# Kernel tuning notes

Hardware: AMD Instinct MI355X
Metric: run time of the kernel (lower is better)

## Reference

```python
import jax, jax.numpy as jnp
import numpy as np
from jax.scipy.stats import norm as jnorm

B, S, D, H, E, K, FF = 8, 256, 1024, 16, 4, 2, 4096
HD = D // H
NOISE_EPS = 0.01
LOSS_COEF = 0.01
EPS_FILL = float(np.finfo(float).eps)


def _ln(x, g, b):
    m = x.mean(-1, keepdims=True)
    v = x.var(-1, keepdims=True)
    return (x - m) * jax.lax.rsqrt(v + 1e-5) * g + b


def setup_inputs() -> dict:
    key = jax.random.key(0)
    ks = jax.random.split(key, 16)
    r = lambda i, shape, s=1.0: jax.random.normal(ks[i], shape, dtype=jnp.float32) * s
    return {
        "x": r(0, (B, S, D)),
        "e_outputs": r(1, (B, 64, D)),            # unused (is_lm=True) but part of signature
        "noise": r(2, (B, E)),                     # the randn_like(clean_logits) draw
        "w_gate": r(3, (D, E), 0.02),
        "w_noise": r(4, (D, E), 0.02),
        "Wq": r(5, (E, D, D), 0.02),
        "Wk": r(6, (E, D, D), 0.02),
        "Wv": r(7, (E, D, D), 0.02),
        "Wo": r(8, (E, D, D), 0.02),
        "W1": r(9, (E, D, FF), 0.02),
        "b1": jnp.zeros((E, FF), jnp.float32),
        "W2": r(10, (E, FF, D), 0.02),
        "b2": jnp.zeros((E, D), jnp.float32),
        "g1": jnp.ones((E, D), jnp.float32),
        "be1": jnp.zeros((E, D), jnp.float32),
        "g2": jnp.ones((E, D), jnp.float32),
        "be2": jnp.zeros((E, D), jnp.float32),
        "trg_mask": jnp.tril(jnp.ones((S, S), dtype=bool))[None, None],  # causal [1,1,S,S]
        "src_mask": jnp.ones((1, 1, 1, 64), dtype=bool),                 # unused (is_lm=True)
    }


def _cv_squared(v):
    # torch .var() is unbiased (ddof=1)
    return v.var(ddof=1) / (v.mean() ** 2 + 1e-10)


def reference(x, e_outputs, noise, w_gate, w_noise, Wq, Wk, Wv, Wo, W1, b1, W2, b2,
              g1, be1, g2, be2, trg_mask, src_mask):
    b, s, d = x.shape
    # ---- noisy top-k gating (per sample, on the sequence-sum) ----
    xs = x.sum(axis=1)                                   # [B, D]
    clean = xs @ w_gate                                  # [B, E]
    raw_noise = xs @ w_noise                             # [B, E]
    stddev = jax.nn.softplus(raw_noise) + NOISE_EPS      # train=True -> *1.0
    noisy = clean + noise * stddev                       # logits
    top_logits, top_idx = jax.lax.top_k(noisy, K + 1)    # [B, K+1]
    topk_gates = jax.nn.softmax(top_logits[:, :K], axis=1)
    gates = jnp.zeros_like(noisy).at[jnp.arange(b)[:, None], top_idx[:, :K]].set(topk_gates)
    # load: prob each expert's clean logit lands in the noisy top-k
    thr_in = top_logits[:, K:K + 1]                      # (k+1)-th noisy value
    thr_out = top_logits[:, K - 1:K]                     # k-th noisy value
    is_in = noisy > thr_in
    prob = jnp.where(is_in,
                     jnorm.cdf((clean - thr_in) / stddev),
                     jnorm.cdf((clean - thr_out) / stddev))
    load = prob.sum(0)                                   # [E]
    importance = gates.sum(0)                            # [E]
    loss = (_cv_squared(importance) + _cv_squared(load)) * LOSS_COEF

    # ---- experts: standard decoder layer (self-attn + FFN), is_lm -> no cross-attn ----
    neg = jnp.asarray(-1e9, x.dtype)
    scale = 1.0 / np.sqrt(HD)

    def expert(p):
        wq, wk, wv, wo, w1, bb1, w2, bb2, gg1, bbe1, gg2, bbe2 = p
        q = (x @ wq).reshape(b, s, H, HD)
        k_ = (x @ wk).reshape(b, s, H, HD)
        v = (x @ wv).reshape(b, s, H, HD)
        scores = jnp.einsum('bqhd,bkhd->bhqk', q, k_) * scale
        scores = jnp.where(trg_mask, scores, neg)
        attn = jax.nn.softmax(scores, axis=-1)
        o = jnp.einsum('bhqk,bkhd->bqhd', attn, v).reshape(b, s, d) @ wo
        h = _ln(x + o, gg1, bbe1)
        ff = jax.nn.relu(h @ w1 + bb1) @ w2 + bb2
        return _ln(h + ff, gg2, bbe2)

    outs = jax.vmap(expert)((Wq, Wk, Wv, Wo, W1, b1, W2, b2, g1, be1, g2, be2))  # [E,B,S,D]

    # ---- combine: scatter-add of gate-weighted expert outputs (dense equivalent) ----
    y = jnp.einsum('be,ebsd->bsd', gates, outs)
    y = jnp.where(y == 0, jnp.asarray(EPS_FILL, y.dtype), y)
    return y, loss
```

## Files before the change

kernel.cpp:

```cpp
#include <hip/hip_runtime.h>
#include <hip/hip_bf16.h>

typedef __bf16 bf16;
typedef __attribute__((ext_vector_type(4))) __bf16 bf16x4;
typedef __attribute__((ext_vector_type(8))) __bf16 bf16x8;
typedef __attribute__((ext_vector_type(4))) float floatx4;

constexpr int CB = 8, CS = 256, CD = 1024, CH = 16, CE = 4, CFF = 4096, CHD = 64;
constexpr long long DD  = 1048576;
constexpr long long DFF = 4194304;
constexpr long long BSD = 2097152;
constexpr long long PSD = 4194304;

constexpr size_t OFF_PART = 0;
constexpr size_t OFF_CLEAN= 262144;
constexpr size_t OFF_RAW  = 262272;
constexpr size_t OFF_GATES= 262400;
constexpr size_t OFF_EACT = 262528;
constexpr size_t OFF_PBE  = 262592;
constexpr size_t OFF_BP   = 262656;
constexpr size_t OFF_XBF  = 263168;
constexpr size_t OFF_WT   = OFF_XBF + (size_t)BSD*2;
constexpr size_t OFF_W1T  = OFF_WT  + (size_t)16*DD*2;
constexpr size_t OFF_W2T  = OFF_W1T + (size_t)4*DFF*2;
constexpr size_t OFF_QKV  = OFF_W2T + (size_t)4*DFF*2;
constexpr size_t OFF_AO   = OFF_QKV + (size_t)3*PSD*2;
constexpr size_t OFF_F1   = OFF_QKV;
constexpr size_t OFF_PB   = OFF_AO  + (size_t)PSD*2;
constexpr size_t OFF_VT   = OFF_PB;
constexpr size_t OFF_H    = OFF_PB  + (size_t)2*PSD*4;
constexpr size_t OFF_HBF  = OFF_H   + (size_t)PSD*4;

__global__ __launch_bounds__(256)
void cvt_xsum(const float* __restrict__ x, bf16* __restrict__ xbf, float* __restrict__ part) {
  int blk = blockIdx.x;
  int b = blk >> 3, ch = blk & 7;
  int t = threadIdx.x;
  float s0 = 0.f, s1 = 0.f, s2 = 0.f, s3 = 0.f;
  long long base4 = ((long long)(b*CS + ch*32))*CD / 4;
#pragma unroll 4
  for (int r = 0; r < 32; ++r) {
    long long i4 = base4 + (long long)r*(CD/4) + t;
    float4 v = ((const float4*)x)[i4];
    bf16x4 o; o[0] = (bf16)v.x; o[1] = (bf16)v.y; o[2] = (bf16)v.z; o[3] = (bf16)v.w;
    ((bf16x4*)xbf)[i4] = o;
    s0 += v.x; s1 += v.y; s2 += v.z; s3 += v.w;
  }
  float4 sv; sv.x = s0; sv.y = s1; sv.z = s2; sv.w = s3;
  ((float4*)(part + (long long)blk*CD))[t] = sv;
}

__global__ __launch_bounds__(256)
void gate_dots(const float* __restrict__ part, const float* __restrict__ wg,
               const float* __restrict__ wn, float* __restrict__ clean, float* __restrict__ raw) {
  int p = blockIdx.x, b = p >> 2, e = p & 3;
  int t = threadIdx.x;
  float s1 = 0.f, s2 = 0.f;
  for (int d = t; d < CD; d += 256) {
    float xv = 0.f;
#pragma unroll
    for (int c = 0; c < 8; ++c) xv += part[(long long)(b*8 + c)*CD + d];
    s1 += xv * wg[d*CE + e];
    s2 += xv * wn[d*CE + e];
  }
  for (int off = 32; off; off >>= 1) { s1 += __shfl_xor(s1, off); s2 += __shfl_xor(s2, off); }
  __shared__ float r1[4], r2[4];
  int lane = t & 63, w = t >> 6;
  if (lane == 0) { r1[w] = s1; r2[w] = s2; }
  __syncthreads();
  if (t == 0) { clean[p] = r1[0]+r1[1]+r1[2]+r1[3]; raw[p] = r2[0]+r2[1]+r2[2]+r2[3]; }
}

__global__ void gating_kernel(const float* __restrict__ clean, const float* __restrict__ raw,
                              const float* __restrict__ noise, float* __restrict__ gates,
                              int* __restrict__ eact, int* __restrict__ pairBE,
                              int* __restrict__ batchPair, float* __restrict__ loss_out) {
  if (threadIdx.x != 0) return;
  float imp[CE] = {0,0,0,0}, load[CE] = {0,0,0,0};
  int act[CE] = {0,0,0,0};
  for (int b = 0; b < CB; ++b) {
    float cl[CE], sd[CE], ny[CE];
    for (int e = 0; e < CE; ++e) {
      cl[e] = clean[b*CE + e];
      float rw = raw[b*CE + e];
      float sp = fmaxf(rw, 0.f) + log1pf(expf(-fabsf(rw)));
      sd[e] = sp + 0.01f;
      ny[e] = cl[e] + noise[b*CE + e]*sd[e];
    }
    int idx[CE] = {0,1,2,3};
    for (int a = 0; a < 3; ++a) {
      int best = a;
      for (int c = a + 1; c < 4; ++c) if (ny[idx[c]] > ny[idx[best]]) best = c;
      int tt = idx[a]; idx[a] = idx[best]; idx[best] = tt;
    }
    float l0 = ny[idx[0]], l1 = ny[idx[1]], l2 = ny[idx[2]];
    float e1 = expf(l1 - l0);
    float g0 = 1.f/(1.f + e1), g1v = e1/(1.f + e1);
    for (int e = 0; e < CE; ++e) gates[b*CE + e] = 0.f;
    gates[b*CE + idx[0]] = g0; gates[b*CE + idx[1]] = g1v;
    imp[idx[0]] += g0; imp[idx[1]] += g1v;
    act[idx[0]] = 1; act[idx[1]] = 1;
    for (int e = 0; e < CE; ++e) {
      bool is_in = ny[e] > l2;
      float thr = is_in ? l2 : l1;
      float zz = (cl[e] - thr) / sd[e];
      load[e] += 0.5f * erfcf(-zz * 0.70710678118654752440f);
    }
  }
  int pe2p[CB][CE];
  int pc = 0;
  for (int e = 0; e < CE; ++e)
    for (int b = 0; b < CB; ++b)
      if (gates[b*CE + e] != 0.f) { pairBE[pc] = b | (e << 8); pe2p[b][e] = pc; ++pc; }
  for (int b = 0; b < CB; ++b) {
    int s = 0;
    for (int e = 0; e < CE; ++e)
      if (gates[b*CE + e] != 0.f) batchPair[2*b + (s++)] = pe2p[b][e];
  }
  float m1 = 0.f, m2 = 0.f;
  for (int e = 0; e < CE; ++e) { m1 += imp[e]; m2 += load[e]; }
  m1 *= 0.25f; m2 *= 0.25f;
  float v1 = 0.f, v2 = 0.f;
  for (int e = 0; e < CE; ++e) { float d1 = imp[e]-m1, d2 = load[e]-m2; v1 += d1*d1; v2 += d2*d2; }
  v1 *= (1.f/3.f); v2 *= (1.f/3.f);
  loss_out[0] = 0.01f * (v1/(m1*m1 + 1e-10f) + v2/(m2*m2 + 1e-10f));
  for (int e = 0; e < CE; ++e) eact[e] = act[e];
}

__global__ __launch_bounds__(256)
void transcvt_all(const float* __restrict__ Wq, const float* __restrict__ Wk,
                  const float* __restrict__ Wv, const float* __restrict__ Wo,
                  const float* __restrict__ W1, const float* __restrict__ W2,
                  bf16* __restrict__ wT, bf16* __restrict__ w1T, bf16* __restrict__ w2T,
                  const int* __restrict__ eact) {
  int z = blockIdx.x;
  const float* src; bf16* d; int rows, cols, tx, ty, e;
  if (z < 8192) {
    int m = z >> 9, t = z & 511; e = m >> 2; int which = m & 3;
    src = ((which == 0) ? Wq : (which == 1) ? Wk : (which == 2) ? Wv : Wo) + (long long)e*DD;
    d = wT + (long long)m*DD; rows = 1024; cols = 1024;
    tx = t & 31; ty = t >> 5;
  } else if (z < 16384) {
    int z2 = z - 8192; e = z2 >> 11; int t = z2 & 2047;
    src = W1 + (long long)e*DFF; d = w1T + (long long)e*DFF;
    rows = 1024; cols = 4096; tx = t & 127; ty = t >> 7;
  } else {
    int z3 = z - 16384; e = z3 >> 11; int t = z3 & 2047;
    src = W2 + (long long)e*DFF; d = w2T + (long long)e*DFF;
    rows = 4096; cols = 1024; tx = t & 31; ty = t >> 5;
  }
  if (eact[e] == 0) return;
  __shared__ float tile[64][33];
  int c0 = tx*32, r0 = ty*64;
  int t = threadIdx.x;
#pragma unroll
  for (int i = 0; i < 8; ++i) {
    int id = i*256 + t; int r = id >> 5, c = id & 31;
    tile[r][c] = src[(long long)(r0 + r)*cols + c0 + c];
  }
  __syncthreads();
  unsigned* dw = (unsigned*)d;
#pragma unroll
  for (int i = 0; i < 4; ++i) {
    int id = i*256 + t; int dr = id >> 5, c = id & 31;
    union { bf16 h[2]; unsigned u; } pk;
    pk.h[0] = (bf16)tile[2*c][dr]; pk.h[1] = (bf16)tile[2*c + 1][dr];
    dw[((long long)(c0 + dr)*rows + r0)/2 + c] = pk.u;
  }
}

__global__ __launch_bounds__(256)
void transpose_v(const bf16* __restrict__ qkvC, bf16* __restrict__ vTb) {
  int z = blockIdx.z; int p = z >> 4, h = z & 15;
  const bf16* v = qkvC + 2*PSD + (long long)(p*CS)*CD + h*CHD;
  bf16* vt = vTb + (long long)(p*CH + h)*CHD*CS;
  __shared__ bf16 tile[32][33];
  int s0 = blockIdx.x*32, d0 = blockIdx.y*32;
  int tx = threadIdx.x % 32, ty = threadIdx.x / 32;
#pragma unroll
  for (int i = 0; i < 4; ++i)
    tile[ty + 8*i][tx] = v[(long long)(s0 + ty + 8*i)*CD + d0 + tx];
  __syncthreads();
#pragma unroll
  for (int i = 0; i < 4; ++i)
    vt[(long long)(d0 + ty + 8*i)*CS + s0 + tx] = tile[tx][ty + 8*i];
}

__device__ __forceinline__ void cp16(const bf16* g, bf16* l) {
  __builtin_amdgcn_global_load_lds((const __attribute__((address_space(1))) void*)g,
                                   (__attribute__((address_space(3))) void*)l, 16, 0, 0);
}

template<int R, int W>
__device__ __forceinline__ void stage(const bf16* __restrict__ src, int ld, bf16* dst) {
  constexpr int W8 = W/8;
  int t = threadIdx.x;
  int l = t & 63, wid = t >> 6;
#pragma unroll
  for (int i = 0; i < (R*W8)/256; ++i) {
    int idb = i*256 + wid*64;
    int id = idb + l;
    int row = id / W8, sl = id % W8;
    int gc = sl ^ (row & 7);
    cp16(src + (long long)row*ld + gc*8, dst + (long long)idb*8);
  }
}

__global__ __launch_bounds__(256)
void attn_fused(const bf16* __restrict__ qkvC, const bf16* __restrict__ vTb,
                bf16* __restrict__ aoC) {
  int h = blockIdx.x, p = blockIdx.y;
  const bf16* qp = qkvC + (long long)(p*CS)*CD + h*CHD;
  const bf16* kp = qp + PSD;
  const bf16* vt = vTb + (long long)(p*CH + h)*CHD*CS;
  bf16* aop = aoC + (long long)(p*CS)*CD + h*CHD;

  __shared__ bf16 Ps[64*264];
  __shared__ float smaxL[64*4], ssumL[64*4], Lrow[64];

  int t = threadIdx.x, w = t >> 6, lane = t & 63, lr = lane & 15, quad = lane >> 4;

  for (int qt = 0; qt < 4; ++qt) {
    floatx4 accs[4][4] = {};
#pragma unroll
    for (int kk = 0; kk < 2; ++kk) {
      int c = kk*4 + quad;
      bf16x8 af[4], bfr[4];
#pragma unroll
      for (int i = 0; i < 4; ++i) {
        af[i]  = *(const bf16x8*)(qp + (long long)(qt*64 + i*16 + lr)*CD + c*8);
        bfr[i] = *(const bf16x8*)(kp + (long long)(w*64  + i*16 + lr)*CD + c*8);
      }
#pragma unroll
      for (int i = 0; i < 4; ++i)
#pragma unroll
        for (int j = 0; j < 4; ++j)
          accs[i][j] = __builtin_amdgcn_mfma_f32_16x16x32_bf16(af[i], bfr[j], accs[i][j], 0, 0, 0);
    }
    float rmax[4][4];
#pragma unroll
    for (int i = 0; i < 4; ++i)
#pragma unroll
      for (int r = 0; r < 4; ++r) {
        int qrow = qt*64 + i*16 + quad*4 + r;
        float m = -3.0e38f;
#pragma unroll
        for (int j = 0; j < 4; ++j) {
          int kcol = w*64 + j*16 + lr;
          float s = accs[i][j][r]*0.125f;
          s = (kcol <= qrow) ? s : -3.0e38f;
          accs[i][j][r] = s;
          m = fmaxf(m, s);
        }
        rmax[i][r] = m;
      }
#pragma unroll
    for (int off = 1; off <= 8; off <<= 1)
#pragma unroll
      for (int i = 0; i < 4; ++i)
#pragma unroll
        for (int r = 0; r < 4; ++r) rmax[i][r] = fmaxf(rmax[i][r], __shfl_xor(rmax[i][r], off));
    if (lr == 0)
#pragma unroll
      for (int i = 0; i < 4; ++i)
#pragma unroll
        for (int r = 0; r < 4; ++r) smaxL[(i*16 + quad*4 + r)*4 + w] = rmax[i][r];
    __syncthreads();
    float rsum[4][4];
#pragma unroll
    for (int i = 0; i < 4; ++i)
#pragma unroll
      for (int r = 0; r < 4; ++r) {
        floatx4 mv = *(const floatx4*)&smaxL[(i*16 + quad*4 + r)*4];
        float M = fmaxf(fmaxf(mv[0], mv[1]), fmaxf(mv[2], mv[3]));
        float srow = 0.f;
#pragma unroll
        for (int j = 0; j < 4; ++j) {
          float pp = __expf(accs[i][j][r] - M);
          accs[i][j][r] = pp;
          srow += pp;
        }
        rsum[i][r] = srow;
      }
#pragma unroll
    for (int off = 1; off <= 8; off <<= 1)
#pragma unroll
      for (int i = 0; i < 4; ++i)
#pragma unroll
        for (int r = 0; r < 4; ++r) rsum[i][r] += __shfl_xor(rsum[i][r], off);
    if (lr == 0)
#pragma unroll
      for (int i = 0; i < 4; ++i)
#pragma unroll
        for (int r = 0; r < 4; ++r) ssumL[(i*16 + quad*4 + r)*4 + w] = rsum[i][r];
    __syncthreads();
    if (w == 0 && lr == 0) {
#pragma unroll
      for (int i = 0; i < 4; ++i)
#pragma unroll
        for (int r = 0; r < 4; ++r) {
          int m = i*16 + quad*4 + r;
          floatx4 sv = *(const floatx4*)&ssumL[m*4];
          Lrow[m] = sv[0] + sv[1] + sv[2] + sv[3];
        }
    }
#pragma unroll
    for (int i = 0; i < 4; ++i)
#pragma unroll
      for (int j = 0; j < 4; ++j)
#pragma unroll
        for (int r = 0; r < 4; ++r)
          Ps[(i*16 + quad*4 + r)*264 + w*64 + j*16 + lr] = (bf16)accs[i][j][r];
    __syncthreads();
    floatx4 acco[4] = {};
#pragma unroll
    for (int ks = 0; ks < 8; ++ks) {
      int c = ks*4 + quad;
      bf16x8 ap = *(const bf16x8*)(Ps + (w*16 + lr)*264 + c*8);
#pragma unroll
      for (int j = 0; j < 4; ++j) {
        bf16x8 bv = *(const bf16x8*)(vt + (long long)(j*16 + lr)*CS + c*8);
        acco[j] = __builtin_amdgcn_mfma_f32_16x16x32_bf16(ap, bv, acco[j], 0, 0, 0);
      }
    }
#pragma unroll
    for (int r = 0; r < 4; ++r) {
      int orow = w*16 + quad*4 + r;
      float inv = 1.f / Lrow[orow];
#pragma unroll
      for (int j = 0; j < 4; ++j)
        aop[(long long)(qt*64 + orow)*CD + j*16 + lr] = (bf16)(acco[j][r]*inv);
    }
    __syncthreads();
  }
}

__global__ __launch_bounds__(256)
void ln1_kernel(const float* __restrict__ x, const float* __restrict__ PbF,
                const float* __restrict__ gamma, const float* __restrict__ beta,
                float* __restrict__ h, bf16* __restrict__ hbf, const int* __restrict__ pairBE) {
  int row = blockIdx.x;
  int pbe = pairBE[row >> 8]; int pb = pbe & 255, pe = pbe >> 8;
  int t = threadIdx.x;
  const float* pa = x + ((long long)pb*CS + (row & 255))*CD;
  const float* p0 = PbF + (long long)row*CD;
  const float* p1 = PbF + PSD + (long long)row*CD;
  const float* gm = gamma + (long long)pe*CD;
  const float* bt = beta  + (long long)pe*CD;
  float v[4]; float s = 0.f, s2 = 0.f;
#pragma unroll
  for (int i = 0; i < 4; ++i) {
    int d = t + 256*i;
    float xv = pa[d] + p0[d] + p1[d];
    v[i] = xv; s += xv; s2 += xv*xv;
  }
  int lane = t & 63, wave = t >> 6;
  for (int off = 32; off; off >>= 1) { s += __shfl_xor(s, off); s2 += __shfl_xor(s2, off); }
  __shared__ float red[8];
  if (lane == 0) { red[wave*2] = s; red[wave*2 + 1] = s2; }
  __syncthreads();
  s  = red[0] + red[2] + red[4] + red[6];
  s2 = red[1] + red[3] + red[5] + red[7];
  float mean = s * (1.f/CD);
  float var  = s2 * (1.f/CD) - mean*mean;
  float rstd = rsqrtf(var + 1e-5f);
#pragma unroll
  for (int i = 0; i < 4; ++i) {
    int d = t + 256*i;
    float val = (v[i] - mean)*rstd*gm[d] + bt[d];
    h  [(long long)row*CD + d] = val;
    hbf[(long long)row*CD + d] = (bf16)val;
  }
}

__global__ __launch_bounds__(256)
void ln2y_kernel(const float* __restrict__ h, const bf16* __restrict__ PbB,
                 const float* __restrict__ gamma, const float* __restrict__ beta,
                 float* __restrict__ y, const float* __restrict__ gates,
                 const int* __restrict__ pairBE, const int* __restrict__ batchPair) {
  int row = blockIdx.x;
  int b = row >> 8, sIdx = row & 255;
  int p0 = batchPair[2*b], p1 = batchPair[2*b + 1];
  int e0 = pairBE[p0] >> 8, e1 = pairBE[p1] >> 8;
  float gv0 = gates[b*CE + e0], gv1 = gates[b*CE + e1];
  long long r0 = (long long)p0*CS + sIdx, r1 = (long long)p1*CS + sIdx;
  int t = threadIdx.x;
  float v0[4], v1[4];
  float sA = 0.f, sA2 = 0.f, sB = 0.f, sB2 = 0.f;
#pragma unroll
  for (int i = 0; i < 4; ++i) {
    int d = t + 256*i;
    float a = h[r0*CD + d];
    float c = h[r1*CD + d];
#pragma unroll
    for (int k = 0; k < 4; ++k) {
      a += (float)PbB[(long long)k*PSD + r0*CD + d];
      c += (float)PbB[(long long)k*PSD + r1*CD + d];
    }
    v0[i] = a; sA += a; sA2 += a*a;
    v1[i] = c; sB += c; sB2 += c*c;
  }
  int lane = t & 63, wave = t >> 6;
  for (int off = 32; off; off >>= 1) {
    sA += __shfl_xor(sA, off); sA2 += __shfl_xor(sA2, off);
    sB += __shfl_xor(sB, off); sB2 += __shfl_xor(sB2, off);
  }
  __shared__ float red[16];
  if (lane == 0) { red[wave*4] = sA; red[wave*4+1] = sA2; red[wave*4+2] = sB; red[wave*4+3] = sB2; }
  __syncthreads();
  sA  = red[0] + red[4] + red[8]  + red[12];
  sA2 = red[1] + red[5] + red[9]  + red[13];
  sB  = red[2] + red[6] + red[10] + red[14];
  sB2 = red[3] + red[7] + red[11] + red[15];
  float mA = sA*(1.f/CD), mB = sB*(1.f/CD);
  float rsA = rsqrtf(sA2*(1.f/CD) - mA*mA + 1e-5f);
  float rsB = rsqrtf(sB2*(1.f/CD) - mB*mB + 1e-5f);
  const float* gm0 = gamma + (long long)e0*CD; const float* bt0 = beta + (long long)e0*CD;
  const float* gm1 = gamma + (long long)e1*CD; const float* bt1 = beta + (long long)e1*CD;
#pragma unroll
  for (int i = 0; i < 4; ++i) {
    int d = t + 256*i;
    float o = gv0*((v0[i] - mA)*rsA*gm0[d] + bt0[d]) + gv1*((v1[i] - mB)*rsB*gm1[d] + bt1[d]);
    y[(long long)row*CD + d] = (o == 0.f) ? 2.2204460492503131e-16f : o;
  }
}

enum { EPI_BF16 = 0, EPI_F32 = 1, EPI_BRELU = 2, EPI_BIASBF16 = 3 };

template<int EPI, int KS, bool A_BATCH>
__global__ __launch_bounds__(256)
void gemm_nt(const bf16* __restrict__ A, const bf16* __restrict__ Bt, void* __restrict__ Cv,
             int K , int lda, int ldb, int ldc,
             long long oBe, long long oBmat, long long oCmat, long long oCk,
             const float* __restrict__ bias, long long biasStride,
             const int* __restrict__ pairBE) {
  constexpr int BM = 128, BN = 128;
  int z = blockIdx.z;
  int zk = z % KS, mat = z / KS;
  int m0 = blockIdx.x * BM, n0 = blockIdx.y * BN;
  int pbe = pairBE[m0 >> 8]; int pb = pbe & 255, pe = pbe >> 8;
  const bf16* Ab = A + (A_BATCH ? ((long long)pb*CS + (m0 & 255))*lda : (long long)m0*lda)
                     + (long long)zk*K;
  const bf16* Bb = Bt + (long long)pe*oBe + (long long)mat*oBmat + (long long)zk*K
                      + (long long)n0*ldb;
  long long coff = (long long)mat*oCmat + (long long)zk*oCk;

  __shared__ bf16 As[BM*64];
  __shared__ bf16 Bs[BN*64];

  int wave = threadIdx.x >> 6;
  int lane = threadIdx.x & 63;
  int wm = wave >> 1, wn = wave & 1;
  int lr = lane & 15;
  int quad = lane >> 4;

  floatx4 acc[4][4] = {};

  for (int kt = 0; kt < K; kt += 64) {
    stage<BM, 64>(Ab + kt, lda, As);
    stage<BN, 64>(Bb + kt, ldb, Bs);
    __syncthreads();
#pragma unroll
    for (int kk = 0; kk < 2; ++kk) {
      bf16x8 af[4], bfr[4];
#pragma unroll
      for (int i = 0; i < 4; ++i) {
        int c = kk*4 + quad;
        int m = wm*64 + i*16 + lr;
        af[i]  = *(const bf16x8*)(As + m*64 + ((c ^ (m & 7))*8));
        int n = wn*64 + i*16 + lr;
        bfr[i] = *(const bf16x8*)(Bs + n*64 + ((c ^ (n & 7))*8));
      }
#pragma unroll
      for (int i = 0; i < 4; ++i)
#pragma unroll
        for (int j = 0; j < 4; ++j)
          acc[i][j] = __builtin_amdgcn_mfma_f32_16x16x32_bf16(af[i], bfr[j], acc[i][j], 0, 0, 0);
    }
    __syncthreads();
  }

#pragma unroll
  for (int j = 0; j < 4; ++j) {
    int col = n0 + wn*64 + j*16 + lr;
    float bv = 0.f;
    if constexpr (EPI == EPI_BRELU || EPI == EPI_BIASBF16)
      if (zk == 0) bv = bias[(long long)pe*biasStride + col];
#pragma unroll
    for (int i = 0; i < 4; ++i) {
#pragma unroll
      for (int r = 0; r < 4; ++r) {
        int row = m0 + wm*64 + i*16 + quad*4 + r;
        float v = acc[i][j][r] + bv;
        long long idx = coff + (long long)row*ldc + col;
        if constexpr (EPI == EPI_BF16)          ((bf16*)Cv)[idx] = (bf16)v;
        else if constexpr (EPI == EPI_F32)      ((float*)Cv)[idx] = v;
        else if constexpr (EPI == EPI_BRELU)    ((bf16*)Cv)[idx] = (bf16)fmaxf(v, 0.f);
        else                                    ((bf16*)Cv)[idx] = (bf16)v;
      }
    }
  }
}

extern "C" void kernel_launch(void* const* d_in, const int* in_sizes, int n_in,
                              void* d_out, int out_size, void* d_ws, size_t ws_size,
                              hipStream_t stream) {
  const float* x       = (const float*)d_in[0];
  const float* noise   = (const float*)d_in[2];
  const float* w_gate  = (const float*)d_in[3];
  const float* w_noise = (const float*)d_in[4];
  const float* Wq      = (const float*)d_in[5];
  const float* Wk      = (const float*)d_in[6];
  const float* Wv      = (const float*)d_in[7];
  const float* Wo      = (const float*)d_in[8];
  const float* W1      = (const float*)d_in[9];
  const float* b1      = (const float*)d_in[10];
  const float* W2      = (const float*)d_in[11];
  const float* b2      = (const float*)d_in[12];
  const float* g1      = (const float*)d_in[13];
  const float* be1     = (const float*)d_in[14];
  const float* g2      = (const float*)d_in[15];
  const float* be2     = (const float*)d_in[16];

  char* ws = (char*)d_ws;
  float* y    = (float*)d_out;
  float* loss = y + (size_t)BSD;

  float* part  = (float*)(ws + OFF_PART);
  float* clean = (float*)(ws + OFF_CLEAN);
  float* raw   = (float*)(ws + OFF_RAW);
  float* gates = (float*)(ws + OFF_GATES);
  int*   eact  = (int*)  (ws + OFF_EACT);
  int*   pairBE= (int*)  (ws + OFF_PBE);
  int*   batchPair = (int*)(ws + OFF_BP);
  bf16*  xbf   = (bf16*) (ws + OFF_XBF);
  bf16*  wT    = (bf16*) (ws + OFF_WT);
  bf16*  w1T   = (bf16*) (ws + OFF_W1T);
  bf16*  w2T   = (bf16*) (ws + OFF_W2T);
  bf16*  qkvC  = (bf16*) (ws + OFF_QKV);
  bf16*  aoC   = (bf16*) (ws + OFF_AO);
  bf16*  f1    = (bf16*) (ws + OFF_F1);
  bf16*  vTb   = (bf16*) (ws + OFF_VT);
  float* PbF   = (float*)(ws + OFF_PB);
  bf16*  PbB   = (bf16*) (ws + OFF_PB);
  float* h     = (float*)(ws + OFF_H);
  bf16*  hbf   = (bf16*) (ws + OFF_HBF);

  cvt_xsum<<<64, 256, 0, stream>>>(x, xbf, part);
  gate_dots<<<32, 256, 0, stream>>>(part, w_gate, w_noise, clean, raw);
  gating_kernel<<<1, 64, 0, stream>>>(clean, raw, noise, gates, eact, pairBE, batchPair, loss);
  transcvt_all<<<24576, 256, 0, stream>>>(Wq, Wk, Wv, Wo, W1, W2, wT, w1T, w2T, eact);

  gemm_nt<EPI_BF16, 1, true><<<dim3(32, 8, 3), 256, 0, stream>>>(
      xbf, wT, qkvC, 1024, 1024, 1024, 1024,
      4*DD, DD, PSD, 0, nullptr, 0, pairBE);

  transpose_v<<<dim3(8, 2, 256), 256, 0, stream>>>(qkvC, vTb);

  attn_fused<<<dim3(CH, 16), 256, 0, stream>>>(qkvC, vTb, aoC);

  gemm_nt<EPI_F32, 2, false><<<dim3(32, 8, 2), 256, 0, stream>>>(
      aoC, wT + 3*DD, PbF, 512, 1024, 1024, 1024,
      4*DD, 0, 0, PSD, nullptr, 0, pairBE);

  ln1_kernel<<<4096, 256, 0, stream>>>(x, PbF, g1, be1, h, hbf, pairBE);

  gemm_nt<EPI_BRELU, 1, false><<<dim3(32, 32, 1), 256, 0, stream>>>(
      hbf, w1T, f1, 1024, 1024, 1024, 4096,
      DFF, 0, 0, 0, b1, CFF, pairBE);

  gemm_nt<EPI_BIASBF16, 4, false><<<dim3(32, 8, 4), 256, 0, stream>>>(
      f1, w2T, PbB, 1024, 4096, 4096, 1024,
      DFF, 0, 0, PSD, b2, CD, pairBE);

  ln2y_kernel<<<2048, 256, 0, stream>>>(h, PbB, g2, be2, y, gates, pairBE, batchPair);
}
```

Before: 526.5 us.

## Vectorize weight transpose, split attention across query tiles, float4 layernorms

The weight transpose-convert kernel now uses 64x64 tiles with float4 loads and 16-byte bf16x8 stores, halving the block count. Attention moves its query-tile loop onto a third grid dimension, giving four times as many blocks, and skips QK and PV work on fully masked causal key tiles. Both layernorm kernels switch to float4 and bf16x4 vector loads and stores. Together these target the bandwidth-bound transpose (likely the largest cost), low occupancy in attention, and scalar memory traffic, at the cost of more LDS per transpose block and wider per-thread loads.

```diff
diff --git a/kernel.cpp b/kernel.cpp
--- a/kernel.cpp
+++ b/kernel.cpp
@@ -134,38 +134,40 @@
                   bf16* __restrict__ wT, bf16* __restrict__ w1T, bf16* __restrict__ w2T,
                   const int* __restrict__ eact) {
   int z = blockIdx.x;
-  const float* src; bf16* d; int rows, cols, tx, ty, e;
-  if (z < 8192) {
-    int m = z >> 9, t = z & 511; e = m >> 2; int which = m & 3;
+  const float* src; bf16* d; int rows, cols, tk, tn, e;
+  if (z < 4096) {
+    int m = z >> 8, tt = z & 255; e = m >> 2; int which = m & 3;
     src = ((which == 0) ? Wq : (which == 1) ? Wk : (which == 2) ? Wv : Wo) + (long long)e*DD;
     d = wT + (long long)m*DD; rows = 1024; cols = 1024;
-    tx = t & 31; ty = t >> 5;
-  } else if (z < 16384) {
-    int z2 = z - 8192; e = z2 >> 11; int t = z2 & 2047;
+    tk = tt >> 4; tn = tt & 15;
+  } else if (z < 8192) {
+    int z2 = z - 4096; e = z2 >> 10; int tt = z2 & 1023;
     src = W1 + (long long)e*DFF; d = w1T + (long long)e*DFF;
-    rows = 1024; cols = 4096; tx = t & 127; ty = t >> 7;
+    rows = 1024; cols = 4096; tk = tt >> 6; tn = tt & 63;
   } else {
-    int z3 = z - 16384; e = z3 >> 11; int t = z3 & 2047;
+    int z3 = z - 8192; e = z3 >> 10; int tt = z3 & 1023;
     src = W2 + (long long)e*DFF; d = w2T + (long long)e*DFF;
-    rows = 4096; cols = 1024; tx = t & 31; ty = t >> 5;
+    rows = 4096; cols = 1024; tk = tt >> 4; tn = tt & 15;
   }
   if (eact[e] == 0) return;
-  __shared__ float tile[64][33];
-  int c0 = tx*32, r0 = ty*64;
+  __shared__ float tile[64][65];
   int t = threadIdx.x;
-#pragma unroll
-  for (int i = 0; i < 8; ++i) {
-    int id = i*256 + t; int r = id >> 5, c = id & 31;
-    tile[r][c] = src[(long long)(r0 + r)*cols + c0 + c];
-  }
-  __syncthreads();
-  unsigned* dw = (unsigned*)d;
+  int k0 = tk*64, n0 = tn*64;
 #pragma unroll
   for (int i = 0; i < 4; ++i) {
-    int id = i*256 + t; int dr = id >> 5, c = id & 31;
-    union { bf16 h[2]; unsigned u; } pk;
-    pk.h[0] = (bf16)tile[2*c][dr]; pk.h[1] = (bf16)tile[2*c + 1][dr];
-    dw[((long long)(c0 + dr)*rows + r0)/2 + c] = pk.u;
+    int id = i*256 + t; int r = id >> 4, c4 = id & 15;
+    float4 v = *(const float4*)&src[(long long)(k0 + r)*cols + n0 + c4*4];
+    tile[r][c4*4 + 0] = v.x; tile[r][c4*4 + 1] = v.y;
+    tile[r][c4*4 + 2] = v.z; tile[r][c4*4 + 3] = v.w;
+  }
+  __syncthreads();
+#pragma unroll
+  for (int i = 0; i < 2; ++i) {
+    int id = i*256 + t; int n = id >> 3, ck = id & 7;
+    bf16x8 o;
+#pragma unroll
+    for (int j = 0; j < 8; ++j) o[j] = (bf16)tile[ck*8 + j][n];
+    *(bf16x8*)&d[(long long)(n0 + n)*rows + k0 + ck*8] = o;
   }
 }
 
@@ -209,7 +211,7 @@
 __global__ __launch_bounds__(256)
 void attn_fused(const bf16* __restrict__ qkvC, const bf16* __restrict__ vTb,
                 bf16* __restrict__ aoC) {
-  int h = blockIdx.x, p = blockIdx.y;
+  int h = blockIdx.x, p = blockIdx.y, qt = blockIdx.z;
   const bf16* qp = qkvC + (long long)(p*CS)*CD + h*CHD;
   const bf16* kp = qp + PSD;
   const bf16* vt = vTb + (long long)(p*CH + h)*CHD*CS;
@@ -220,8 +222,8 @@
 
   int t = threadIdx.x, w = t >> 6, lane = t & 63, lr = lane & 15, quad = lane >> 4;
 
-  for (int qt = 0; qt < 4; ++qt) {
-    floatx4 accs[4][4] = {};
+  floatx4 accs[4][4] = {};
+  if (w <= qt) {
 #pragma unroll
     for (int kk = 0; kk < 2; ++kk) {
       int c = kk*4 + quad;
@@ -237,73 +239,75 @@
         for (int j = 0; j < 4; ++j)
           accs[i][j] = __builtin_amdgcn_mfma_f32_16x16x32_bf16(af[i], bfr[j], accs[i][j], 0, 0, 0);
     }
-    float rmax[4][4];
+  }
+  float rmax[4][4];
+#pragma unroll
+  for (int i = 0; i < 4; ++i)
+#pragma unroll
+    for (int r = 0; r < 4; ++r) {
+      int qrow = qt*64 + i*16 + quad*4 + r;
+      float m = -3.0e38f;
+#pragma unroll
+      for (int j = 0; j < 4; ++j) {
+        int kcol = w*64 + j*16 + lr;
+        float s = accs[i][j][r]*0.125f;
+        s = (kcol <= qrow) ? s : -3.0e38f;
+        accs[i][j][r] = s;
+        m = fmaxf(m, s);
+      }
+      rmax[i][r] = m;
+    }
+#pragma unroll
+  for (int off = 1; off <= 8; off <<= 1)
 #pragma unroll
     for (int i = 0; i < 4; ++i)
 #pragma unroll
+      for (int r = 0; r < 4; ++r) rmax[i][r] = fmaxf(rmax[i][r], __shfl_xor(rmax[i][r], off));
+  if (lr == 0)
+#pragma unroll
+    for (int i = 0; i < 4; ++i)
+#pragma unroll
+      for (int r = 0; r < 4; ++r) smaxL[(i*16 + quad*4 + r)*4 + w] = rmax[i][r];
+  __syncthreads();
+  float rsum[4][4];
+#pragma unroll
+  for (int i = 0; i < 4; ++i)
+#pragma unroll
+    for (int r = 0; r < 4; ++r) {
+      floatx4 mv = *(const floatx4*)&smaxL[(i*16 + quad*4 + r)*4];
+      float M = fmaxf(fmaxf(mv[0], mv[1]), fmaxf(mv[2], mv[3]));
+      float srow = 0.f;
+#pragma unroll
+      for (int j = 0; j < 4; ++j) {
+        float pp = __expf(accs[i][j][r] - M);
+        accs[i][j][r] = pp;
+        srow += pp;
+      }
+      rsum[i][r] = srow;
+    }
+#pragma unroll
+  for (int off = 1; off <= 8; off <<= 1)
+#pragma unroll
+    for (int i = 0; i < 4; ++i)
+#pragma unroll
+      for (int r = 0; r < 4; ++r) rsum[i][r] += __shfl_xor(rsum[i][r], off);
+  if (lr == 0)
+#pragma unroll
+    for (int i = 0; i < 4; ++i)
+#pragma unroll
+      for (int r = 0; r < 4; ++r) ssumL[(i*16 + quad*4 + r)*4 + w] = rsum[i][r];
+  __syncthreads();
+  if (w == 0 && lr == 0) {
+#pragma unroll
+    for (int i = 0; i < 4; ++i)
+#pragma unroll
       for (int r = 0; r < 4; ++r) {
-        int qrow = qt*64 + i*16 + quad*4 + r;
-        float m = -3.0e38f;
-#pragma unroll
-        for (int j = 0; j < 4; ++j) {
-          int kcol = w*64 + j*16 + lr;
-          float s = accs[i][j][r]*0.125f;
-          s = (kcol <= qrow) ? s : -3.0e38f;
-          accs[i][j][r] = s;
-          m = fmaxf(m, s);
-        }
-        rmax[i][r] = m;
+        int m = i*16 + quad*4 + r;
+        floatx4 sv = *(const floatx4*)&ssumL[m*4];
+        Lrow[m] = sv[0] + sv[1] + sv[2] + sv[3];
       }
-#pragma unroll
-    for (int off = 1; off <= 8; off <<= 1)
-#pragma unroll
-      for (int i = 0; i < 4; ++i)
-#pragma unroll
-        for (int r = 0; r < 4; ++r) rmax[i][r] = fmaxf(rmax[i][r], __shfl_xor(rmax[i][r], off));
-    if (lr == 0)
-#pragma unroll
-      for (int i = 0; i < 4; ++i)
-#pragma unroll
-        for (int r = 0; r < 4; ++r) smaxL[(i*16 + quad*4 + r)*4 + w] = rmax[i][r];
-    __syncthreads();
-    float rsum[4][4];
-#pragma unroll
-    for (int i = 0; i < 4; ++i)
-#pragma unroll
-      for (int r = 0; r < 4; ++r) {
-        floatx4 mv = *(const floatx4*)&smaxL[(i*16 + quad*4 + r)*4];
-        float M = fmaxf(fmaxf(mv[0], mv[1]), fmaxf(mv[2], mv[3]));
-        float srow = 0.f;
-#pragma unroll
-        for (int j = 0; j < 4; ++j) {
-          float pp = __expf(accs[i][j][r] - M);
-          accs[i][j][r] = pp;
-          srow += pp;
-        }
-        rsum[i][r] = srow;
-      }
-#pragma unroll
-    for (int off = 1; off <= 8; off <<= 1)
-#pragma unroll
-      for (int i = 0; i < 4; ++i)
-#pragma unroll
-        for (int r = 0; r < 4; ++r) rsum[i][r] += __shfl_xor(rsum[i][r], off);
-    if (lr == 0)
-#pragma unroll
-      for (int i = 0; i < 4; ++i)
-#pragma unroll
-        for (int r = 0; r < 4; ++r) ssumL[(i*16 + quad*4 + r)*4 + w] = rsum[i][r];
-    __syncthreads();
-    if (w == 0 && lr == 0) {
-#pragma unroll
-      for (int i = 0; i < 4; ++i)
-#pragma unroll
-        for (int r = 0; r < 4; ++r) {
-          int m = i*16 + quad*4 + r;
-          floatx4 sv = *(const floatx4*)&ssumL[m*4];
-          Lrow[m] = sv[0] + sv[1] + sv[2] + sv[3];
-        }
-    }
+  }
+  if (w <= qt) {
 #pragma unroll
     for (int i = 0; i < 4; ++i)
 #pragma unroll
@@ -311,27 +315,26 @@
 #pragma unroll
         for (int r = 0; r < 4; ++r)
           Ps[(i*16 + quad*4 + r)*264 + w*64 + j*16 + lr] = (bf16)accs[i][j][r];
-    __syncthreads();
-    floatx4 acco[4] = {};
-#pragma unroll
-    for (int ks = 0; ks < 8; ++ks) {
-      int c = ks*4 + quad;
-      bf16x8 ap = *(const bf16x8*)(Ps + (w*16 + lr)*264 + c*8);
-#pragma unroll
-      for (int j = 0; j < 4; ++j) {
-        bf16x8 bv = *(const bf16x8*)(vt + (long long)(j*16 + lr)*CS + c*8);
-        acco[j] = __builtin_amdgcn_mfma_f32_16x16x32_bf16(ap, bv, acco[j], 0, 0, 0);
-      }
-    }
-#pragma unroll
-    for (int r = 0; r < 4; ++r) {
-      int orow = w*16 + quad*4 + r;
-      float inv = 1.f / Lrow[orow];
-#pragma unroll
-      for (int j = 0; j < 4; ++j)
-        aop[(long long)(qt*64 + orow)*CD + j*16 + lr] = (bf16)(acco[j][r]*inv);
-    }
-    __syncthreads();
+  }
+  __syncthreads();
+  floatx4 acco[4] = {};
+  int ksMax = (qt + 1)*2;
+  for (int ks = 0; ks < ksMax; ++ks) {
+    int c = ks*4 + quad;
+    bf16x8 ap = *(const bf16x8*)(Ps + (w*16 + lr)*264 + c*8);
+#pragma unroll
+    for (int j = 0; j < 4; ++j) {
+      bf16x8 bv = *(const bf16x8*)(vt + (long long)(j*16 + lr)*CS + c*8);
+      acco[j] = __builtin_amdgcn_mfma_f32_16x16x32_bf16(ap, bv, acco[j], 0, 0, 0);
+    }
+  }
+#pragma unroll
+  for (int r = 0; r < 4; ++r) {
+    int orow = w*16 + quad*4 + r;
+    float inv = 1.f / Lrow[orow];
+#pragma unroll
+    for (int j = 0; j < 4; ++j)
+      aop[(long long)(qt*64 + orow)*CD + j*16 + lr] = (bf16)(acco[j][r]*inv);
   }
 }
 
@@ -342,18 +345,13 @@
   int row = blockIdx.x;
   int pbe = pairBE[row >> 8]; int pb = pbe & 255, pe = pbe >> 8;
   int t = threadIdx.x;
-  const float* pa = x + ((long long)pb*CS + (row & 255))*CD;
-  const float* p0 = PbF + (long long)row*CD;
-  const float* p1 = PbF + PSD + (long long)row*CD;
-  const float* gm = gamma + (long long)pe*CD;
-  const float* bt = beta  + (long long)pe*CD;
-  float v[4]; float s = 0.f, s2 = 0.f;
-#pragma unroll
-  for (int i = 0; i < 4; ++i) {
-    int d = t + 256*i;
-    float xv = pa[d] + p0[d] + p1[d];
-    v[i] = xv; s += xv; s2 += xv*xv;
-  }
+  float4 a = ((const float4*)(x + ((long long)pb*CS + (row & 255))*CD))[t];
+  float4 b = ((const float4*)(PbF + (long long)row*CD))[t];
+  float4 c = ((const float4*)(PbF + PSD + (long long)row*CD))[t];
+  float v0 = a.x + b.x + c.x, v1 = a.y + b.y + c.y;
+  float v2 = a.z + b.z + c.z, v3 = a.w + b.w + c.w;
+  float s  = v0 + v1 + v2 + v3;
+  float s2 = v0*v0 + v1*v1 + v2*v2 + v3*v3;
   int lane = t & 63, wave = t >> 6;
   for (int off = 32; off; off >>= 1) { s += __shfl_xor(s, off); s2 += __shfl_xor(s2, off); }
   __shared__ float red[8];
@@ -362,15 +360,17 @@
   s  = red[0] + red[2] + red[4] + red[6];
   s2 = red[1] + red[3] + red[5] + red[7];
   float mean = s * (1.f/CD);
-  float var  = s2 * (1.f/CD) - mean*mean;
-  float rstd = rsqrtf(var + 1e-5f);
-#pragma unroll
-  for (int i = 0; i < 4; ++i) {
-    int d = t + 256*i;
-    float val = (v[i] - mean)*rstd*gm[d] + bt[d];
-    h  [(long long)row*CD + d] = val;
-    hbf[(long long)row*CD + d] = (bf16)val;
-  }
+  float rstd = rsqrtf(s2*(1.f/CD) - mean*mean + 1e-5f);
+  float4 gm = ((const float4*)(gamma + (long long)pe*CD))[t];
+  float4 bt = ((const float4*)(beta  + (long long)pe*CD))[t];
+  float4 o;
+  o.x = (v0 - mean)*rstd*gm.x + bt.x;
+  o.y = (v1 - mean)*rstd*gm.y + bt.y;
+  o.z = (v2 - mean)*rstd*gm.z + bt.z;
+  o.w = (v3 - mean)*rstd*gm.w + bt.w;
+  ((float4*)(h + (long long)row*CD))[t] = o;
+  bf16x4 ob; ob[0] = (bf16)o.x; ob[1] = (bf16)o.y; ob[2] = (bf16)o.z; ob[3] = (bf16)o.w;
+  ((bf16x4*)(hbf + (long long)row*CD))[t] = ob;
 }
 
 __global__ __launch_bounds__(256)
@@ -385,21 +385,19 @@
   float gv0 = gates[b*CE + e0], gv1 = gates[b*CE + e1];
   long long r0 = (long long)p0*CS + sIdx, r1 = (long long)p1*CS + sIdx;
   int t = threadIdx.x;
-  float v0[4], v1[4];
-  float sA = 0.f, sA2 = 0.f, sB = 0.f, sB2 = 0.f;
-#pragma unroll
-  for (int i = 0; i < 4; ++i) {
-    int d = t + 256*i;
-    float a = h[r0*CD + d];
-    float c = h[r1*CD + d];
-#pragma unroll
-    for (int k = 0; k < 4; ++k) {
-      a += (float)PbB[(long long)k*PSD + r0*CD + d];
-      c += (float)PbB[(long long)k*PSD + r1*CD + d];
-    }
-    v0[i] = a; sA += a; sA2 += a*a;
-    v1[i] = c; sB += c; sB2 += c*c;
-  }
+  float4 a = ((const float4*)(h + r0*CD))[t];
+  float4 c = ((const float4*)(h + r1*CD))[t];
+#pragma unroll
+  for (int k = 0; k < 4; ++k) {
+    bf16x4 pa = ((const bf16x4*)(PbB + (long long)k*PSD + r0*CD))[t];
+    bf16x4 pc = ((const bf16x4*)(PbB + (long long)k*PSD + r1*CD))[t];
+    a.x += (float)pa[0]; a.y += (float)pa[1]; a.z += (float)pa[2]; a.w += (float)pa[3];
+    c.x += (float)pc[0]; c.y += (float)pc[1]; c.z += (float)pc[2]; c.w += (float)pc[3];
+  }
+  float sA = a.x + a.y + a.z + a.w;
+  float sA2 = a.x*a.x + a.y*a.y + a.z*a.z + a.w*a.w;
+  float sB = c.x + c.y + c.z + c.w;
+  float sB2 = c.x*c.x + c.y*c.y + c.z*c.z + c.w*c.w;
   int lane = t & 63, wave = t >> 6;
   for (int off = 32; off; off >>= 1) {
     sA += __shfl_xor(sA, off); sA2 += __shfl_xor(sA2, off);
@@ -415,14 +413,19 @@
   float mA = sA*(1.f/CD), mB = sB*(1.f/CD);
   float rsA = rsqrtf(sA2*(1.f/CD) - mA*mA + 1e-5f);
   float rsB = rsqrtf(sB2*(1.f/CD) - mB*mB + 1e-5f);
-  const float* gm0 = gamma + (long long)e0*CD; const float* bt0 = beta + (long long)e0*CD;
-  const float* gm1 = gamma + (long long)e1*CD; const float* bt1 = beta + (long long)e1*CD;
-#pragma unroll
-  for (int i = 0; i < 4; ++i) {
-    int d = t + 256*i;
-    float o = gv0*((v0[i] - mA)*rsA*gm0[d] + bt0[d]) + gv1*((v1[i] - mB)*rsB*gm1[d] + bt1[d]);
-    y[(long long)row*CD + d] = (o == 0.f) ? 2.2204460492503131e-16f : o;
-  }
+  float4 gm0 = ((const float4*)(gamma + (long long)e0*CD))[t];
+  float4 bt0 = ((const float4*)(beta  + (long long)e0*CD))[t];
+  float4 gm1 = ((const float4*)(gamma + (long long)e1*CD))[t];
+  float4 bt1 = ((const float4*)(beta  + (long long)e1*CD))[t];
+  float4 o;
+  o.x = gv0*((a.x - mA)*rsA*gm0.x + bt0.x) + gv1*((c.x - mB)*rsB*gm1.x + bt1.x);
+  o.y = gv0*((a.y - mA)*rsA*gm0.y + bt0.y) + gv1*((c.y - mB)*rsB*gm1.y + bt1.y);
+  o.z = gv0*((a.z - mA)*rsA*gm0.z + bt0.z) + gv1*((c.z - mB)*rsB*gm1.z + bt1.z);
+  o.w = gv0*((a.w - mA)*rsA*gm0.w + bt0.w) + gv1*((c.w - mB)*rsB*gm1.w + bt1.w);
+  constexpr float EF = 2.2204460492503131e-16f;
+  o.x = (o.x == 0.f) ? EF : o.x;  o.y = (o.y == 0.f) ? EF : o.y;
+  o.z = (o.z == 0.f) ? EF : o.z;  o.w = (o.w == 0.f) ? EF : o.w;
+  ((float4*)(y + (long long)row*CD))[t] = o;
 }
 
 enum { EPI_BF16 = 0, EPI_F32 = 1, EPI_BRELU = 2, EPI_BIASBF16 = 3 };
@@ -549,7 +552,7 @@
   cvt_xsum<<<64, 256, 0, stream>>>(x, xbf, part);
   gate_dots<<<32, 256, 0, stream>>>(part, w_gate, w_noise, clean, raw);
   gating_kernel<<<1, 64, 0, stream>>>(clean, raw, noise, gates, eact, pairBE, batchPair, loss);
-  transcvt_all<<<24576, 256, 0, stream>>>(Wq, Wk, Wv, Wo, W1, W2, wT, w1T, w2T, eact);
+  transcvt_all<<<12288, 256, 0, stream>>>(Wq, Wk, Wv, Wo, W1, W2, wT, w1T, w2T, eact);
 
   gemm_nt<EPI_BF16, 1, true><<<dim3(32, 8, 3), 256, 0, stream>>>(
       xbf, wT, qkvC, 1024, 1024, 1024, 1024,
@@ -557,7 +560,7 @@
 
   transpose_v<<<dim3(8, 2, 256), 256, 0, stream>>>(qkvC, vTb);
 
-  attn_fused<<<dim3(CH, 16), 256, 0, stream>>>(qkvC, vTb, aoC);
+  attn_fused<<<dim3(CH, 16, 4), 256, 0, stream>>>(qkvC, vTb, aoC);
 
   gemm_nt<EPI_F32, 2, false><<<dim3(32, 8, 2), 256, 0, stream>>>(
       aoC, wT + 3*DD, PbF, 512, 1024, 1024, 1024,
```

Measured after the change: 518.8 us. Within noise of the previous version (-1.5%).
